# Kernel optimization log

Measured on AMD Instinct MI355X. Metric: run time of the kernel, lower is better.

## Reference

```python
import jax, jax.numpy as jnp
import numpy as np

S = 2048      # seq_len
H = 32        # num_heads
G = 8         # num_groups (KV heads)
D = 128       # head_dim
HPG = H // G  # heads per group
MODEL = H * D


def setup_inputs() -> dict:
    rng = jax.random.key(0)
    ks = jax.random.split(rng, 6)
    return {
        "query": jax.random.normal(ks[0], (S, H, D), jnp.float32),
        "key":   jax.random.normal(ks[1], (S, G, D), jnp.float32),
        "value": jax.random.normal(ks[2], (S, G, D), jnp.float32),
        "mask":  jnp.zeros((S, S), jnp.float32),
        "w_out": jax.random.normal(ks[3], (MODEL, MODEL), jnp.float32) * (MODEL ** -0.5),
        "b_out": jnp.zeros((MODEL,), jnp.float32),
    }


def reference(query, key, value, mask, w_out, b_out):
    # NOTE: the original torch module prepares `mask` but never applies it to
    # the attention scores; we faithfully reproduce that (mask is unused).
    scale = D ** -0.5
    # [S,H,D] -> [H,S,D] -> [G,HPG,S,D]; head h = g*HPG + i (torch .view split)
    q = query.transpose(1, 0, 2).reshape(G, HPG, S, D)
    k = key.transpose(1, 0, 2)    # [G,S,D]
    v = value.transpose(1, 0, 2)  # [G,S,D]
    scores = jnp.einsum('ghqd,gkd->ghqk', q, k) * scale  # [G,HPG,S,S]
    attn = jax.nn.softmax(scores, axis=-1)
    out = jnp.einsum('ghqk,gkd->ghqd', attn, v)          # [G,HPG,S,D]
    # [G,HPG,S,D] -> [H,S,D] -> [S,H,D] -> [S, H*D]
    out = out.reshape(H, S, D).transpose(1, 0, 2).reshape(S, MODEL)
    out = out @ w_out.T + b_out                           # out_proj (Linear)
    return out.reshape(S, H, D)
```

## Files before the change

### kernel.cpp

```cpp
#include <hip/hip_runtime.h>
#include <hip/hip_bf16.h>
#include <stdint.h>

constexpr int S_ = 2048, H_ = 32, G_ = 8, HPG_ = 4, D_ = 128, MODEL_ = 4096;

typedef __attribute__((ext_vector_type(4))) float f32x4;
typedef __attribute__((ext_vector_type(16))) float f32x16;
typedef __attribute__((ext_vector_type(8))) short bf16x8;
typedef __attribute__((ext_vector_type(4))) short bf16x4;

__device__ inline unsigned short f2bf(float f) {
  unsigned u = __float_as_uint(f);
  u += 0x7FFFu + ((u >> 16) & 1u);
  return (unsigned short)(u >> 16);
}

__device__ inline unsigned cvt_pk_bf16(float lo, float hi) {
  unsigned r;
  asm("v_cvt_pk_bf16_f32 %0, %1, %2" : "=v"(r) : "v"(lo), "v"(hi));
  return r;
}

__device__ inline void gload_lds16(const void* g, void* l) {
  __builtin_amdgcn_global_load_lds(
      (const __attribute__((address_space(1))) unsigned int*)g,
      (__attribute__((address_space(3))) unsigned int*)l,
      16, 0, 0);
}

__global__ __launch_bounds__(256) void cvt_f32_to_bf16(
    const float* __restrict__ in, unsigned short* __restrict__ out, int n4) {
  int i = blockIdx.x * 256 + threadIdx.x;
  if (i < n4) {
    float4 v = reinterpret_cast<const float4*>(in)[i];
    bf16x4 o;
    o[0] = f2bf(v.x); o[1] = f2bf(v.y); o[2] = f2bf(v.z); o[3] = f2bf(v.w);
    reinterpret_cast<bf16x4*>(out)[i] = o;
  }
}

__global__ __launch_bounds__(256) void cvt_k_kernel(
    const float* __restrict__ in, unsigned short* __restrict__ out) {
  int i = blockIdx.x * 256 + threadIdx.x;
  int d4 = i & 31, g = (i >> 5) & 7, s = i >> 8;
  float4 v = reinterpret_cast<const float4*>(in)[i];
  bf16x4 o;
  o[0] = f2bf(v.x); o[1] = f2bf(v.y); o[2] = f2bf(v.z); o[3] = f2bf(v.w);
  reinterpret_cast<bf16x4*>(out)[(g * S_ + s) * 32 + d4] = o;
}

__global__ __launch_bounds__(256) void cvt_v_kernel(
    const float* __restrict__ in, unsigned short* __restrict__ out) {
  __shared__ float t[64][33];
  int s0 = blockIdx.x * 64, d0 = blockIdx.y * 32, g = blockIdx.z;
  int tid = threadIdx.x;
#pragma unroll
  for (int p = 0; p < 2; ++p) {
    int idx = p * 256 + tid;
    int s = idx >> 3, dq = (idx & 7) * 4;
    float4 v = *reinterpret_cast<const float4*>(
        in + ((size_t)(s0 + s) * G_ + g) * D_ + d0 + dq);
    t[s][dq] = v.x; t[s][dq + 1] = v.y; t[s][dq + 2] = v.z; t[s][dq + 3] = v.w;
  }
  __syncthreads();
  int d = tid >> 3, sq = (tid & 7) * 8;
  bf16x8 o;
#pragma unroll
  for (int j = 0; j < 8; ++j) o[j] = f2bf(t[sq + j][d]);
  *reinterpret_cast<bf16x8*>(out + ((size_t)g * D_ + d0 + d) * S_ + s0 + sq) = o;
}

constexpr int QB2 = 128, KVB = 32, NT = S_ / KVB;
constexpr float RTHR = 8.0f;

__global__ __launch_bounds__(256, 2) void attn32_kernel(
    const float* __restrict__ q, const unsigned short* __restrict__ kb,
    const unsigned short* __restrict__ vtb, unsigned short* __restrict__ aout) {
  __shared__ __align__(16) char smem[49152];

  const int qt = blockIdx.x, h = blockIdx.y;
  const int g = h >> 2;
  const int tid = threadIdx.x, w = tid >> 6, lane = tid & 63;
  const int l31 = lane & 31, hi = lane >> 5;

  const float scale = 0.08838834764831845f;
  bf16x8 qf[8];
  const int qrow = qt * QB2 + w * 32 + l31;
  {
    const float* qp = q + ((size_t)qrow * H_ + h) * D_;
#pragma unroll
    for (int c = 0; c < 8; ++c) {
      const float* p0 = qp + c * 16 + hi * 8;
      float4 a = *(const float4*)p0;
      float4 b = *(const float4*)(p0 + 4);
      bf16x8 f;
      f[0] = f2bf(a.x * scale); f[1] = f2bf(a.y * scale);
      f[2] = f2bf(a.z * scale); f[3] = f2bf(a.w * scale);
      f[4] = f2bf(b.x * scale); f[5] = f2bf(b.y * scale);
      f[6] = f2bf(b.z * scale); f[7] = f2bf(b.w * scale);
      qf[c] = f;
    }
  }

  int ks_kv[2], ks_d[2], vs_d[2], vs_kv[2];
#pragma unroll
  for (int hh = 0; hh < 2; ++hh) {
    int p = w * 1024 + hh * 4096 + lane * 16;
    int kvr = p >> 8;
    ks_kv[hh] = kvr;
    ks_d[hh] = ((p & 255) ^ ((kvr & 7) << 4)) >> 1;
    int dr = p >> 6;
    vs_d[hh] = dr;
    vs_kv[hh] = ((p & 63) ^ (((dr >> 1) & 3) << 4)) >> 1;
  }
  const unsigned short* kg = kb + (size_t)g * S_ * D_;
  const unsigned short* vg = vtb + (size_t)g * D_ * S_;

  auto stage = [&](int t, int buf) {
    int kv0 = t * KVB;
    char* Kd = smem + buf * 16384;
    char* Vd = smem + buf * 16384 + 8192;
#pragma unroll
    for (int hh = 0; hh < 2; ++hh) {
      gload_lds16(kg + (size_t)(kv0 + ks_kv[hh]) * D_ + ks_d[hh],
                  Kd + w * 1024 + hh * 4096);
      gload_lds16(vg + (size_t)vs_d[hh] * S_ + kv0 + vs_kv[hh],
                  Vd + w * 1024 + hh * 4096);
    }
  };

  f32x16 of[4];
#pragma unroll
  for (int i = 0; i < 4; ++i) of[i] = (f32x16)0.f;
  float m = -1e30f, l = 0.f;

  stage(0, 0);
  stage(1, 1);

  for (int t = 0; t < NT; ++t) {
    const int buf = t % 3;
    if (t + 1 < NT) asm volatile("s_waitcnt vmcnt(4)" ::: "memory");
    else            asm volatile("s_waitcnt vmcnt(0)" ::: "memory");
    __builtin_amdgcn_s_barrier();
    if (t + 2 < NT) stage(t + 2, (t + 2) % 3);

    const char* Kd = smem + buf * 16384;
    const char* Vd = smem + buf * 16384 + 8192;

    f32x16 s0 = (f32x16)0.f, s1 = (f32x16)0.f;
    __builtin_amdgcn_s_setprio(1);
#pragma unroll
    for (int c = 0; c < 8; ++c) {
      unsigned off = ((unsigned)(l31 * 256 + c * 32 + hi * 16)) ^
                     ((unsigned)(l31 & 7) << 4);
      bf16x8 kf = *(const bf16x8*)(Kd + off);
      if (c & 1)
        s1 = __builtin_amdgcn_mfma_f32_32x32x16_bf16(kf, qf[c], s1, 0, 0, 0);
      else
        s0 = __builtin_amdgcn_mfma_f32_32x32x16_bf16(kf, qf[c], s0, 0, 0, 0);
    }
    __builtin_amdgcn_s_setprio(0);
    f32x16 sv = s0 + s1;

    float tmax = sv[0];
#pragma unroll
    for (int r = 1; r < 16; ++r) tmax = fmaxf(tmax, sv[r]);
    tmax = fmaxf(tmax, __shfl_xor(tmax, 32));
    if (__any(tmax > m + RTHR)) {
      float mnew = fmaxf(m, tmax);
      float alpha = __expf(m - mnew);
#pragma unroll
      for (int i = 0; i < 4; ++i)
#pragma unroll
        for (int r = 0; r < 16; ++r) of[i][r] *= alpha;
      l *= alpha;
      m = mnew;
    }
    float pv[16];
    float sum = 0.f;
#pragma unroll
    for (int r = 0; r < 16; ++r) { pv[r] = __expf(sv[r] - m); sum += pv[r]; }
    sum += __shfl_xor(sum, 32);
    l += sum;

    unsigned pk[8];
#pragma unroll
    for (int b = 0; b < 8; ++b) pk[b] = cvt_pk_bf16(pv[2 * b], pv[2 * b + 1]);
    bf16x8 pf[2];
#pragma unroll
    for (int kc = 0; kc < 2; ++kc) {
      auto sA = __builtin_amdgcn_permlane32_swap(pk[kc * 4 + 0], pk[kc * 4 + 2],
                                                 false, false);
      auto sB = __builtin_amdgcn_permlane32_swap(pk[kc * 4 + 1], pk[kc * 4 + 3],
                                                 false, false);
      unsigned fr[4] = {(unsigned)sA[0], (unsigned)sB[0],
                        (unsigned)sA[1], (unsigned)sB[1]};
      __builtin_memcpy(&pf[kc], fr, 16);
    }

    __builtin_amdgcn_s_setprio(1);
#pragma unroll
    for (int db = 0; db < 4; ++db) {
      int d = db * 32 + l31;
#pragma unroll
      for (int kc = 0; kc < 2; ++kc) {
        unsigned off = ((unsigned)(d * 64 + kc * 32 + hi * 16)) ^
                       ((unsigned)((d >> 1) & 3) << 4);
        bf16x8 vf = *(const bf16x8*)(Vd + off);
        of[db] = __builtin_amdgcn_mfma_f32_32x32x16_bf16(vf, pf[kc], of[db], 0, 0, 0);
      }
    }
    __builtin_amdgcn_s_setprio(0);
  }

  __syncthreads();
  float inv = 1.0f / l;
  unsigned short* Ol = (unsigned short*)smem;
  const int ql = w * 32 + l31;
#pragma unroll
  for (int db = 0; db < 4; ++db) {
#pragma unroll
    for (int rp = 0; rp < 8; ++rp) {
      int r0 = rp * 2;
      int d0 = db * 32 + (r0 & 3) + 8 * (r0 >> 2) + 4 * hi;
      unsigned pkv = cvt_pk_bf16(of[db][r0] * inv, of[db][r0 + 1] * inv);
      unsigned off = ((unsigned)(ql * 256 + d0 * 2)) ^ ((unsigned)(ql & 7) << 4);
      *(unsigned*)((char*)Ol + off) = pkv;
    }
  }
  __syncthreads();
  const size_t obase = ((size_t)qt * QB2) * MODEL_ + (size_t)h * D_;
#pragma unroll
  for (int pass = 0; pass < 8; ++pass) {
    int row = pass * 16 + (tid >> 4);
    int c = tid & 15;
    unsigned off = ((unsigned)(row * 256 + c * 16)) ^ ((unsigned)(row & 7) << 4);
    bf16x8 vv = *(const bf16x8*)((char*)Ol + off);
    *(bf16x8*)(aout + obase + (size_t)row * MODEL_ + c * 8) = vv;
  }
}

constexpr int BM = 128, BN = 128, BK = 64;

__global__ __launch_bounds__(256, 2) void gemm_bt_bias(
    const unsigned short* __restrict__ A, const unsigned short* __restrict__ B,
    const float* __restrict__ bias, float* __restrict__ C) {
  __shared__ unsigned short As[BM * BK];
  __shared__ unsigned short Bs[BN * BK];

  const int tid = threadIdx.x;
  const int w = tid >> 6, lane = tid & 63;
  const int wr = w >> 1, wc = w & 1;
  const int r16 = lane & 15, g4 = lane >> 4;
  const int row0 = blockIdx.y * BM, col0 = blockIdx.x * BN;

  f32x4 acc[4][4];
#pragma unroll
  for (int m = 0; m < 4; ++m)
#pragma unroll
    for (int n = 0; n < 4; ++n) acc[m][n] = (f32x4)0.f;

  for (int kt = 0; kt < MODEL_ / BK; ++kt) {
    const int k0 = kt * BK;
    __syncthreads();
#pragma unroll
    for (int j = 0; j < 4; ++j) {
      int chunk = w * 4 + j;
      int sb = chunk * 1024 + lane * 16;
      int srow = sb >> 7;
      int lb = sb ^ ((srow & 7) << 4);
      int kk = (lb & 127) >> 1;
      gload_lds16(A + (size_t)(row0 + srow) * MODEL_ + k0 + kk,
                  (char*)As + chunk * 1024);
      gload_lds16(B + (size_t)(col0 + srow) * MODEL_ + k0 + kk,
                  (char*)Bs + chunk * 1024);
    }
    asm volatile("s_waitcnt vmcnt(0)" ::: "memory");
    __syncthreads();

#pragma unroll
    for (int kc = 0; kc < 2; ++kc) {
      bf16x8 af[4], bfr[4];
#pragma unroll
      for (int m = 0; m < 4; ++m) {
        int row = wr * 64 + m * 16 + r16;
        unsigned off = ((unsigned)(row * 128 + (kc * 32 + g4 * 8) * 2)) ^ ((row & 7) << 4);
        af[m] = *(bf16x8*)((char*)As + off);
      }
#pragma unroll
      for (int n = 0; n < 4; ++n) {
        int row = wc * 64 + n * 16 + r16;
        unsigned off = ((unsigned)(row * 128 + (kc * 32 + g4 * 8) * 2)) ^ ((row & 7) << 4);
        bfr[n] = *(bf16x8*)((char*)Bs + off);
      }
#pragma unroll
      for (int m = 0; m < 4; ++m)
#pragma unroll
        for (int n = 0; n < 4; ++n)
          acc[m][n] = __builtin_amdgcn_mfma_f32_16x16x32_bf16(af[m], bfr[n], acc[m][n], 0, 0, 0);
    }
  }

#pragma unroll
  for (int n = 0; n < 4; ++n) {
    int col = col0 + wc * 64 + n * 16 + r16;
    float bv = bias[col];
#pragma unroll
    for (int m = 0; m < 4; ++m) {
      int rbase = row0 + wr * 64 + m * 16 + g4 * 4;
#pragma unroll
      for (int j = 0; j < 4; ++j)
        C[(size_t)(rbase + j) * MODEL_ + col] = acc[m][n][j] + bv;
    }
  }
}

extern "C" void kernel_launch(void* const* d_in, const int* in_sizes, int n_in,
                              void* d_out, int out_size, void* d_ws, size_t ws_size,
                              hipStream_t stream) {
  const float* q = (const float*)d_in[0];
  const float* k = (const float*)d_in[1];
  const float* v = (const float*)d_in[2];
  const float* w_out = (const float*)d_in[4];
  const float* b_out = (const float*)d_in[5];
  float* out = (float*)d_out;

  unsigned short* attn_bf = (unsigned short*)d_ws;
  unsigned short* xreg = attn_bf + (size_t)S_ * MODEL_;
  unsigned short* k_bf = xreg;
  unsigned short* vt_bf = xreg + (size_t)G_ * S_ * D_;
  unsigned short* w_bf = xreg;
  if (ws_size < ((size_t)S_ * MODEL_ + (size_t)MODEL_ * MODEL_) * 2) return;

  cvt_k_kernel<<<S_ * G_ * D_ / 4 / 256, 256, 0, stream>>>(k, k_bf);
  dim3 vg(S_ / 64, D_ / 32, G_);
  cvt_v_kernel<<<vg, 256, 0, stream>>>(v, vt_bf);

  dim3 ag(S_ / QB2, H_);
  attn32_kernel<<<ag, 256, 0, stream>>>(q, k_bf, vt_bf, attn_bf);

  cvt_f32_to_bf16<<<(MODEL_ * MODEL_ / 4) / 256, 256, 0, stream>>>(
      w_out, w_bf, MODEL_ * MODEL_ / 4);

  dim3 gg(MODEL_ / BN, S_ / BM);
  gemm_bt_bias<<<gg, 256, 0, stream>>>(attn_bf, w_bf, b_out, out);
}
```

Baseline: 185.5 us.

## Raise attention occupancy, use exp2 softmax, new LDS swizzles, remap GEMM blocks

Several independent changes: the attention kernel's launch bound goes from 2 to 3 blocks per CU. Q is pre-scaled by log2(e)/sqrt(D) so softmax can use exp2 instead of expf, and the max reduction becomes a tree. Staging precomputes global pointers, and the K and V LDS layouts get new XOR swizzles (V now uses 256-byte rows) to cut address math and bank conflicts. The GEMM launches a 1D grid with blocks remapped across XCDs for L2 locality. The tighter register budget at 3 blocks per CU risks spills, and with 48KB of LDS per block three blocks may not fit on a CU anyway.

New measurement: 192.7 us. 1.04x slower.

```diff
diff --git a/kernel.cpp b/kernel.cpp
--- a/kernel.cpp
+++ b/kernel.cpp
@@ -73,7 +73,7 @@
 constexpr int QB2 = 128, KVB = 32, NT = S_ / KVB;
 constexpr float RTHR = 8.0f;
 
-__global__ __launch_bounds__(256, 2) void attn32_kernel(
+__global__ __launch_bounds__(256, 3) void attn32_kernel(
     const float* __restrict__ q, const unsigned short* __restrict__ kb,
     const unsigned short* __restrict__ vtb, unsigned short* __restrict__ aout) {
   __shared__ __align__(16) char smem[49152];
@@ -83,10 +83,10 @@
   const int tid = threadIdx.x, w = tid >> 6, lane = tid & 63;
   const int l31 = lane & 31, hi = lane >> 5;
 
-  const float scale = 0.08838834764831845f;
+  const float scale2 = 0.12751742354783493f;
   bf16x8 qf[8];
-  const int qrow = qt * QB2 + w * 32 + l31;
   {
+    const int qrow = qt * QB2 + w * 32 + l31;
     const float* qp = q + ((size_t)qrow * H_ + h) * D_;
 #pragma unroll
     for (int c = 0; c < 8; ++c) {
@@ -94,38 +94,37 @@
       float4 a = *(const float4*)p0;
       float4 b = *(const float4*)(p0 + 4);
       bf16x8 f;
-      f[0] = f2bf(a.x * scale); f[1] = f2bf(a.y * scale);
-      f[2] = f2bf(a.z * scale); f[3] = f2bf(a.w * scale);
-      f[4] = f2bf(b.x * scale); f[5] = f2bf(b.y * scale);
-      f[6] = f2bf(b.z * scale); f[7] = f2bf(b.w * scale);
+      f[0] = f2bf(a.x * scale2); f[1] = f2bf(a.y * scale2);
+      f[2] = f2bf(a.z * scale2); f[3] = f2bf(a.w * scale2);
+      f[4] = f2bf(b.x * scale2); f[5] = f2bf(b.y * scale2);
+      f[6] = f2bf(b.z * scale2); f[7] = f2bf(b.w * scale2);
       qf[c] = f;
     }
   }
 
-  int ks_kv[2], ks_d[2], vs_d[2], vs_kv[2];
-#pragma unroll
-  for (int hh = 0; hh < 2; ++hh) {
-    int p = w * 1024 + hh * 4096 + lane * 16;
-    int kvr = p >> 8;
-    ks_kv[hh] = kvr;
-    ks_d[hh] = ((p & 255) ^ ((kvr & 7) << 4)) >> 1;
-    int dr = p >> 6;
-    vs_d[hh] = dr;
-    vs_kv[hh] = ((p & 63) ^ (((dr >> 1) & 3) << 4)) >> 1;
-  }
-  const unsigned short* kg = kb + (size_t)g * S_ * D_;
-  const unsigned short* vg = vtb + (size_t)g * D_ * S_;
-
-  auto stage = [&](int t, int buf) {
+  const unsigned short* pK[2];
+  const unsigned short* pV[2];
+  {
+    const unsigned short* kg = kb + (size_t)g * S_ * D_;
+    const unsigned short* vg = vtb + (size_t)g * D_ * S_;
+#pragma unroll
+    for (int j = 0; j < 2; ++j) {
+      int p = (w * 2 + j) * 1024 + lane * 16;
+      int kvr = p >> 8;
+      pK[j] = kg + (size_t)kvr * D_ + (((p & 255) ^ ((kvr & 15) << 4)) >> 1);
+      int R = p >> 8;
+      int il = (p & 255) ^ ((R & 7) << 4);
+      pV[j] = vg + (size_t)(R * 4 + (il >> 6)) * S_ + ((il & 63) >> 1);
+    }
+  }
+
+  auto stage = [&](int t) {
     int kv0 = t * KVB;
-    char* Kd = smem + buf * 16384;
-    char* Vd = smem + buf * 16384 + 8192;
-#pragma unroll
-    for (int hh = 0; hh < 2; ++hh) {
-      gload_lds16(kg + (size_t)(kv0 + ks_kv[hh]) * D_ + ks_d[hh],
-                  Kd + w * 1024 + hh * 4096);
-      gload_lds16(vg + (size_t)vs_d[hh] * S_ + kv0 + vs_kv[hh],
-                  Vd + w * 1024 + hh * 4096);
+    char* base = smem + (t % 3) * 16384;
+#pragma unroll
+    for (int j = 0; j < 2; ++j) {
+      gload_lds16(pK[j] + (size_t)kv0 * D_, base + (w * 2 + j) * 1024);
+      gload_lds16(pV[j] + kv0, base + 8192 + (w * 2 + j) * 1024);
     }
   };
 
@@ -134,25 +133,24 @@
   for (int i = 0; i < 4; ++i) of[i] = (f32x16)0.f;
   float m = -1e30f, l = 0.f;
 
-  stage(0, 0);
-  stage(1, 1);
+  stage(0);
+  stage(1);
 
   for (int t = 0; t < NT; ++t) {
-    const int buf = t % 3;
     if (t + 1 < NT) asm volatile("s_waitcnt vmcnt(4)" ::: "memory");
     else            asm volatile("s_waitcnt vmcnt(0)" ::: "memory");
     __builtin_amdgcn_s_barrier();
-    if (t + 2 < NT) stage(t + 2, (t + 2) % 3);
-
-    const char* Kd = smem + buf * 16384;
-    const char* Vd = smem + buf * 16384 + 8192;
+    if (t + 2 < NT) stage(t + 2);
+
+    const char* Kd = smem + (t % 3) * 16384;
+    const char* Vd = Kd + 8192;
 
     f32x16 s0 = (f32x16)0.f, s1 = (f32x16)0.f;
     __builtin_amdgcn_s_setprio(1);
 #pragma unroll
     for (int c = 0; c < 8; ++c) {
-      unsigned off = ((unsigned)(l31 * 256 + c * 32 + hi * 16)) ^
-                     ((unsigned)(l31 & 7) << 4);
+      unsigned off = (unsigned)(l31 * 256) +
+                     (((unsigned)(c * 32 + hi * 16)) ^ ((unsigned)(l31 & 15) << 4));
       bf16x8 kf = *(const bf16x8*)(Kd + off);
       if (c & 1)
         s1 = __builtin_amdgcn_mfma_f32_32x32x16_bf16(kf, qf[c], s1, 0, 0, 0);
@@ -162,13 +160,15 @@
     __builtin_amdgcn_s_setprio(0);
     f32x16 sv = s0 + s1;
 
-    float tmax = sv[0];
-#pragma unroll
-    for (int r = 1; r < 16; ++r) tmax = fmaxf(tmax, sv[r]);
+    float tmax = fmaxf(
+        fmaxf(fmaxf(fmaxf(sv[0], sv[8]), fmaxf(sv[4], sv[12])),
+              fmaxf(fmaxf(sv[1], sv[9]), fmaxf(sv[5], sv[13]))),
+        fmaxf(fmaxf(fmaxf(sv[2], sv[10]), fmaxf(sv[6], sv[14])),
+              fmaxf(fmaxf(sv[3], sv[11]), fmaxf(sv[7], sv[15]))));
     tmax = fmaxf(tmax, __shfl_xor(tmax, 32));
     if (__any(tmax > m + RTHR)) {
       float mnew = fmaxf(m, tmax);
-      float alpha = __expf(m - mnew);
+      float alpha = __builtin_exp2f(m - mnew);
 #pragma unroll
       for (int i = 0; i < 4; ++i)
 #pragma unroll
@@ -176,16 +176,18 @@
       l *= alpha;
       m = mnew;
     }
-    float pv[16];
+    unsigned pk[8];
     float sum = 0.f;
 #pragma unroll
-    for (int r = 0; r < 16; ++r) { pv[r] = __expf(sv[r] - m); sum += pv[r]; }
+    for (int b = 0; b < 8; ++b) {
+      float p0 = __builtin_exp2f(sv[2 * b] - m);
+      float p1 = __builtin_exp2f(sv[2 * b + 1] - m);
+      sum += p0 + p1;
+      pk[b] = cvt_pk_bf16(p0, p1);
+    }
     sum += __shfl_xor(sum, 32);
     l += sum;
 
-    unsigned pk[8];
-#pragma unroll
-    for (int b = 0; b < 8; ++b) pk[b] = cvt_pk_bf16(pv[2 * b], pv[2 * b + 1]);
     bf16x8 pf[2];
 #pragma unroll
     for (int kc = 0; kc < 2; ++kc) {
@@ -201,11 +203,12 @@
     __builtin_amdgcn_s_setprio(1);
 #pragma unroll
     for (int db = 0; db < 4; ++db) {
-      int d = db * 32 + l31;
+      int R = db * 8 + (l31 >> 2);
+      unsigned lg = (unsigned)((l31 & 3) * 64);
 #pragma unroll
       for (int kc = 0; kc < 2; ++kc) {
-        unsigned off = ((unsigned)(d * 64 + kc * 32 + hi * 16)) ^
-                       ((unsigned)((d >> 1) & 3) << 4);
+        unsigned off = (unsigned)(R * 256) +
+                       ((lg + (unsigned)(kc * 32 + hi * 16)) ^ ((unsigned)(R & 7) << 4));
         bf16x8 vf = *(const bf16x8*)(Vd + off);
         of[db] = __builtin_amdgcn_mfma_f32_32x32x16_bf16(vf, pf[kc], of[db], 0, 0, 0);
       }
@@ -252,7 +255,9 @@
   const int w = tid >> 6, lane = tid & 63;
   const int wr = w >> 1, wc = w & 1;
   const int r16 = lane & 15, g4 = lane >> 4;
-  const int row0 = blockIdx.y * BM, col0 = blockIdx.x * BN;
+  const int id = blockIdx.x;
+  const int lin = (id & 7) * 64 + (id >> 3);
+  const int row0 = (lin & 15) * BM, col0 = (lin >> 4) * BN;
 
   f32x4 acc[4][4];
 #pragma unroll
@@ -342,6 +347,5 @@
   cvt_f32_to_bf16<<<(MODEL_ * MODEL_ / 4) / 256, 256, 0, stream>>>(
       w_out, w_bf, MODEL_ * MODEL_ / 4);
 
-  dim3 gg(MODEL_ / BN, S_ / BM);
-  gemm_bt_bias<<<gg, 256, 0, stream>>>(attn_bf, w_bf, b_out, out);
-}
+  gemm_bt_bias<<<512, 256, 0, stream>>>(attn_bf, w_bf, b_out, out);
+}
```
